# Kernel optimization log

Measured on AMD Instinct MI355X. Metric: run time of the kernel, lower is better.

The kernel has to match this reference:

```python
import jax, jax.numpy as jnp
import numpy as np

N, D, K = 131072, 128, 256
MAX_ITER = 8
TOL = 1e-4


def setup_inputs() -> dict:
    key = jax.random.key(0)
    kx, kp = jax.random.split(key)
    X = jax.random.normal(kx, (N, D), dtype=jnp.float32)
    # torch.randperm(N)[:K] -> distinct initial centroid indices
    init_idx = jax.random.permutation(kp, N)[:K]
    return {"X": X, "init_idx": init_idx, "max_iter": MAX_ITER}


def _assign(X, centroids):
    # argmin over Euclidean distance == argmin over squared distance;
    # ||x||^2 is constant per row so drop it: d2[n,k] = ||c_k||^2 - 2 x_n . c_k
    d2 = jnp.sum(centroids * centroids, axis=1)[None, :] - 2.0 * (X @ centroids.T)  # [N,K]
    return jnp.argmin(d2, axis=1)  # [N]


def reference(X, init_idx, max_iter):
    n = X.shape[0]
    centroids0 = X[init_idx]  # [K,D]

    def step(carry, _):
        centroids, done = carry
        labels = _assign(X, centroids)  # [N]
        sums = jax.ops.segment_sum(X, labels, num_segments=K)  # [K,D]
        counts = jax.ops.segment_sum(jnp.ones((n,), X.dtype), labels, num_segments=K)  # [K]
        new_c = sums / counts[:, None]  # empty cluster -> 0/0 = nan (matches torch mean of empty)
        shift = jnp.linalg.norm(new_c - centroids)
        new_done = jnp.logical_or(done, shift < TOL)
        # torch breaks BEFORE assigning new centroids when converged
        centroids = jnp.where(new_done, centroids, new_c)
        return (centroids, new_done), labels

    (centroids, _), labels_hist = jax.lax.scan(
        step, (centroids0, jnp.array(False)), None, length=max_iter
    )
    labels = labels_hist[-1]
    return labels, centroids
```

## Files before the change

### kernel.cpp

```cpp
#include <hip/hip_runtime.h>

#define NP 131072
#define DD 128
#define KK 256
#define MAXIT 8
#define TOLSQ (1e-4f * 1e-4f)
#define POSB 256
#define UPIPE 8

typedef _Float16 half8 __attribute__((ext_vector_type(8)));
typedef float f32x4 __attribute__((ext_vector_type(4)));

__device__ __forceinline__ void async_copy16(const void* g, void* l) {
    __builtin_amdgcn_global_load_lds(
        (const __attribute__((address_space(1))) void*)g,
        (__attribute__((address_space(3))) void*)l, 16, 0, 0);
}

struct Ws {
    float C[KK * DD];
    float newC[KK * DD];
    float cnorm[KK];
    float sums[KK * DD];
    float shiftsq;
    int done;
    int ilab[NP];
    int counts[KK];
    int cursor[KK];
    int ordlab[NP];
    alignas(16) _Float16 Csh[KK * DD];
    alignas(16) _Float16 Csl[KK * DD];
    alignas(16) _Float16 Xsh[(size_t)NP * DD];
    alignas(16) _Float16 Xsl[(size_t)NP * DD];
};

__global__ void k_init(const float* __restrict__ X, const int* __restrict__ idx,
                       float* __restrict__ C, int* __restrict__ done) {
    int k = blockIdx.x, d = threadIdx.x;
    C[k * DD + d] = X[(size_t)idx[k] * DD + d];
    if (k == 0 && d == 0) *done = 0;
}

__global__ void k_split(const float* __restrict__ X, _Float16* __restrict__ Xh,
                        _Float16* __restrict__ Xl) {
    size_t idx = (size_t)blockIdx.x * 256 + threadIdx.x;
    int lane = idx & 63;
    size_t g16k = idx >> 6;
    size_t point = (g16k >> 2) * 16 + (lane & 15);
    int dim0 = (int)(g16k & 3) * 32 + (lane >> 4) * 8;
    const f32x4* s4 = (const f32x4*)(X + point * DD + dim0);
    f32x4 a = s4[0], b = s4[1];
    half8 h, l;
#pragma unroll
    for (int j = 0; j < 4; j++) {
        _Float16 hi = (_Float16)a[j];
        h[j] = hi; l[j] = (_Float16)(a[j] - (float)hi);
    }
#pragma unroll
    for (int j = 0; j < 4; j++) {
        _Float16 hi = (_Float16)b[j];
        h[4 + j] = hi; l[4 + j] = (_Float16)(b[j] - (float)hi);
    }
    *(half8*)(Xh + idx * 8) = h;
    *(half8*)(Xl + idx * 8) = l;
}

__global__ void k_prep0(const float* __restrict__ C, float* __restrict__ cnorm,
                        _Float16* __restrict__ Ch, _Float16* __restrict__ Cl,
                        int* __restrict__ counts, int* __restrict__ cursor) {
    int k = blockIdx.x, d = threadIdx.x;
    float v = C[k * DD + d];
    _Float16 hi = (_Float16)v;
    int ct = k >> 4, l4 = k & 15, ks = d >> 5, q = (d >> 3) & 3, j = d & 7;
    size_t dst = ((size_t)(ks * 16 + ct) * 64 + (q * 16 + l4)) * 8 + j;
    Ch[dst] = hi;
    Cl[dst] = (_Float16)(v - (float)hi);
    __shared__ float red[DD];
    red[d] = v * v;
    __syncthreads();
    for (int s = DD / 2; s > 0; s >>= 1) {
        if (d < s) red[d] += red[d + s];
        __syncthreads();
    }
    if (d == 0) {
        cnorm[k] = red[0];
        counts[k] = 0;
        cursor[k] = 0;
    }
}

__global__ __launch_bounds__(512, 2) void k_assign(
    const _Float16* __restrict__ Xh, const _Float16* __restrict__ Xl,
    const _Float16* __restrict__ Ch, const _Float16* __restrict__ Cl,
    const float* __restrict__ cnorm, float* __restrict__ outlab,
    int* __restrict__ ilab, int* __restrict__ counts,
    float* __restrict__ shiftsq) {
    __shared__ __align__(16) _Float16 B[2 * KK * DD];
    __shared__ int hist[KK];
    const int tid = threadIdx.x;
    const int wave = tid >> 6;
    const int lane = tid & 63;
    const int l4 = lane & 15, g = lane >> 4;

    if (blockIdx.x == 0 && tid == 0) *shiftsq = 0.0f;
    if (tid < KK) hist[tid] = 0;

    char* const lds = (char*)B;
#pragma unroll
    for (int r = 0; r < 8; r++) {
        const int slot = r * 512 + wave * 64;
        async_copy16(Ch + (size_t)(slot + lane) * 8, lds + (size_t)slot * 16);
        async_copy16(Cl + (size_t)(slot + lane) * 8,
                     lds + 65536 + (size_t)slot * 16);
    }

    float cn[16];
#pragma unroll
    for (int ct = 0; ct < 16; ct++) cn[ct] = cnorm[ct * 16 + l4];

    __syncthreads();

#pragma unroll 1
    for (int t = 0; t < 2; t++) {
        const int g16 = blockIdx.x * 32 + t * 16 + wave * 2;

        f32x4 acc[2][16];
#pragma unroll
        for (int pg = 0; pg < 2; pg++)
#pragma unroll
            for (int ct = 0; ct < 16; ct++) acc[pg][ct] = (f32x4){0.f, 0.f, 0.f, 0.f};

        size_t a0 = ((size_t)(g16 * 4 + 0) * 64 + lane) * 8;
        size_t a1 = ((size_t)((g16 + 1) * 4 + 0) * 64 + lane) * 8;
        half8 ah0 = *(const half8*)(Xh + a0);
        half8 al0 = *(const half8*)(Xl + a0);
        half8 ah1 = *(const half8*)(Xh + a1);
        half8 al1 = *(const half8*)(Xl + a1);

#pragma unroll 1
        for (int ks = 0; ks < 4; ks++) {
            half8 nh0, nl0, nh1, nl1;
            if (ks < 3) {
                const size_t b0 = ((size_t)(g16 * 4 + ks + 1) * 64 + lane) * 8;
                const size_t b1 = ((size_t)((g16 + 1) * 4 + ks + 1) * 64 + lane) * 8;
                nh0 = *(const half8*)(Xh + b0);
                nl0 = *(const half8*)(Xl + b0);
                nh1 = *(const half8*)(Xh + b1);
                nl1 = *(const half8*)(Xl + b1);
            }

            char* const curh = lds + ks * 16384;
            char* const curl = lds + 65536 + ks * 16384;
#pragma unroll
            for (int ct = 0; ct < 16; ct++) {
                half8 bh = *(const half8*)(curh + ct * 1024 + lane * 16);
                half8 bl = *(const half8*)(curl + ct * 1024 + lane * 16);
                acc[0][ct] = __builtin_amdgcn_mfma_f32_16x16x32_f16(al0, bh, acc[0][ct], 0, 0, 0);
                acc[0][ct] = __builtin_amdgcn_mfma_f32_16x16x32_f16(ah0, bl, acc[0][ct], 0, 0, 0);
                acc[0][ct] = __builtin_amdgcn_mfma_f32_16x16x32_f16(ah0, bh, acc[0][ct], 0, 0, 0);
                acc[1][ct] = __builtin_amdgcn_mfma_f32_16x16x32_f16(al1, bh, acc[1][ct], 0, 0, 0);
                acc[1][ct] = __builtin_amdgcn_mfma_f32_16x16x32_f16(ah1, bl, acc[1][ct], 0, 0, 0);
                acc[1][ct] = __builtin_amdgcn_mfma_f32_16x16x32_f16(ah1, bh, acc[1][ct], 0, 0, 0);
            }
            ah0 = nh0; al0 = nl0; ah1 = nh1; al1 = nl1;
        }

        unsigned long long best[2][4];
#pragma unroll
        for (int pg = 0; pg < 2; pg++)
#pragma unroll
            for (int r = 0; r < 4; r++) best[pg][r] = ~0ull;

#pragma unroll
        for (int pg = 0; pg < 2; pg++)
#pragma unroll
            for (int ct = 0; ct < 16; ct++)
#pragma unroll
                for (int r = 0; r < 4; r++) {
                    float s = fmaf(-2.0f, acc[pg][ct][r], cn[ct]);
                    if (__builtin_isnan(s)) s = -__builtin_inff();
                    unsigned u = __float_as_uint(s);
                    unsigned m = (u >> 31) ? ~u : (u ^ 0x80000000u);
                    unsigned long long key =
                        ((unsigned long long)m << 32) | (unsigned)(ct * 16 + l4);
                    if (key < best[pg][r]) best[pg][r] = key;
                }

#pragma unroll
        for (int d = 1; d < 16; d <<= 1)
#pragma unroll
            for (int pg = 0; pg < 2; pg++)
#pragma unroll
                for (int r = 0; r < 4; r++) {
                    unsigned long long o = __shfl_xor(best[pg][r], d, 64);
                    if (o < best[pg][r]) best[pg][r] = o;
                }

        if (l4 == 0) {
#pragma unroll
            for (int pg = 0; pg < 2; pg++)
#pragma unroll
                for (int r = 0; r < 4; r++) {
                    int point = (g16 + pg) * 16 + g * 4 + r;
                    int lbl = (int)(best[pg][r] & 0x1ff);
                    outlab[point] = (float)lbl;
                    ilab[point] = lbl;
                    atomicAdd(&hist[lbl], 1);
                }
        }
    }

    __syncthreads();
    if (tid < KK) {
        int h = hist[tid];
        if (h) atomicAdd(&counts[tid], h);
    }
}

__global__ __launch_bounds__(256) void k_scatter(
    const int* __restrict__ ilab, const int* __restrict__ counts,
    int* __restrict__ cursor, int* __restrict__ ordlab,
    float* __restrict__ sums) {
    const int t = threadIdx.x;
    const int b = blockIdx.x;

    if (t < 128) sums[b * 128 + t] = 0.0f;

    __shared__ int hist[KK];
    __shared__ int pre[KK];
    __shared__ int gbase[KK];
    hist[t] = 0;
    int c = counts[t];
    pre[t] = c;
    __syncthreads();

    const int p0 = b * 512;
    const int la = ilab[p0 + t];
    const int lb = ilab[p0 + 256 + t];
    atomicAdd(&hist[la], 1);
    atomicAdd(&hist[lb], 1);

#pragma unroll
    for (int d = 1; d < KK; d <<= 1) {
        int v = (t >= d) ? pre[t - d] : 0;
        __syncthreads();
        pre[t] += v;
        __syncthreads();
    }
    int h = hist[t];
    int gb = (pre[t] - c) + (h ? atomicAdd(&cursor[t], h) : 0);
    gbase[t] = gb;
    __syncthreads();
    hist[t] = 0;
    __syncthreads();

    int ra = atomicAdd(&hist[la], 1);
    ordlab[gbase[la] + ra] = (p0 + t) | (la << 17);
    int rb = atomicAdd(&hist[lb], 1);
    ordlab[gbase[lb] + rb] = (p0 + 256 + t) | (lb << 17);
}

__global__ __launch_bounds__(256) void k_sum(
    const float* __restrict__ X, const int* __restrict__ ordlab,
    float* __restrict__ sums) {
    const int t = threadIdx.x;
    const int d = t & 127, h = t >> 7;

    __shared__ int sol[POSB];
    sol[t] = ordlab[blockIdx.x * POSB + t];
    __syncthreads();

    const int PP = POSB / 2;
    float xv[UPIPE], xn[UPIPE];
#pragma unroll
    for (int u = 0; u < UPIPE; u++)
        xv[u] = X[(size_t)(sol[2 * u + h] & 0x1ffff) * DD + d];

    float acc = 0.0f;
    int cur = sol[h] >> 17;

    for (int jb = 0; jb < PP; jb += UPIPE) {
#pragma unroll
        for (int u = 0; u < UPIPE; u++) {
            int nj = jb + u + UPIPE;
            int o = sol[2 * (nj < PP ? nj : PP - 1) + h];
            xn[u] = X[(size_t)(o & 0x1ffff) * DD + d];
        }
#pragma unroll
        for (int u = 0; u < UPIPE; u++) {
            int l = sol[2 * (jb + u) + h] >> 17;
            if (l != cur) {
                atomicAdd(&sums[cur * DD + d], acc);
                acc = 0.0f;
                cur = l;
            }
            acc += xv[u];
        }
#pragma unroll
        for (int u = 0; u < UPIPE; u++) xv[u] = xn[u];
    }
    atomicAdd(&sums[cur * DD + d], acc);
}

__global__ void k_reduce(const float* __restrict__ sums, const int* __restrict__ counts,
                         const float* __restrict__ C, float* __restrict__ newC,
                         float* __restrict__ shiftsq) {
    const int g = blockIdx.x * 256 + threadIdx.x;
    const int k = g >> 7;
    const int t = threadIdx.x;

    float nc = sums[g] / (float)counts[k];
    newC[g] = nc;
    float diff = nc - C[g];

    __shared__ float red[256];
    red[t] = diff * diff;
    __syncthreads();
    for (int st = 128; st > 0; st >>= 1) {
        if (t < st) red[t] += red[t + st];
        __syncthreads();
    }
    if (t == 0) atomicAdd(shiftsq, red[0]);
}

__global__ void k_upprep(const float* __restrict__ newC, float* __restrict__ C,
                         const float* __restrict__ shiftsq, int* __restrict__ done,
                         float* __restrict__ cnorm, _Float16* __restrict__ Ch,
                         _Float16* __restrict__ Cl, int* __restrict__ counts,
                         int* __restrict__ cursor) {
    const int t = threadIdx.x;
    const int k = blockIdx.x * 2 + (t >> 7);
    const int d = t & 127;
    float ss = *shiftsq;
    int nd = (*done != 0) || (ss < TOLSQ);
    float v = nd ? C[k * DD + d] : newC[k * DD + d];
    C[k * DD + d] = v;
    if (blockIdx.x == 0 && t == 0 && nd) *done = 1;
    if (d == 0) {
        counts[k] = 0;
        cursor[k] = 0;
    }

    _Float16 hi = (_Float16)v;
    int ct = k >> 4, l4 = k & 15, ks = d >> 5, q = (d >> 3) & 3, j = d & 7;
    size_t dst = ((size_t)(ks * 16 + ct) * 64 + (q * 16 + l4)) * 8 + j;
    Ch[dst] = hi;
    Cl[dst] = (_Float16)(v - (float)hi);

    __shared__ float red[256];
    red[t] = v * v;
    __syncthreads();
    for (int s = 64; s > 0; s >>= 1) {
        if ((t & 127) < s) red[t] += red[t + s];
        __syncthreads();
    }
    if (d == 0) cnorm[k] = red[t];
}

__global__ void k_final(const float* __restrict__ C, float* __restrict__ out) {
    int i = blockIdx.x * 256 + threadIdx.x;
    out[i] = C[i];
}

extern "C" void kernel_launch(void* const* d_in, const int* in_sizes, int n_in,
                              void* d_out, int out_size, void* d_ws, size_t ws_size,
                              hipStream_t stream) {
    const float* X = (const float*)d_in[0];
    const int* idx = (const int*)d_in[1];
    float* out = (float*)d_out;
    Ws* w = (Ws*)d_ws;

    k_init<<<KK, DD, 0, stream>>>(X, idx, w->C, &w->done);
    k_split<<<(int)((size_t)NP * DD / 8 / 256), 256, 0, stream>>>(X, w->Xsh, w->Xsl);
    k_prep0<<<KK, DD, 0, stream>>>(w->C, w->cnorm, w->Csh, w->Csl, w->counts, w->cursor);

    for (int it = 0; it < MAXIT; it++) {
        k_assign<<<NP / 512, 512, 0, stream>>>(w->Xsh, w->Xsl, w->Csh, w->Csl,
                                               w->cnorm, out, w->ilab, w->counts,
                                               &w->shiftsq);
        k_scatter<<<NP / 512, 256, 0, stream>>>(w->ilab, w->counts, w->cursor,
                                                w->ordlab, w->sums);
        k_sum<<<NP / POSB, 256, 0, stream>>>(X, w->ordlab, w->sums);
        k_reduce<<<KK * DD / 256, 256, 0, stream>>>(w->sums, w->counts, w->C,
                                                    w->newC, &w->shiftsq);
        k_upprep<<<KK / 2, 256, 0, stream>>>(w->newC, w->C, &w->shiftsq, &w->done,
                                             w->cnorm, w->Csh, w->Csl, w->counts,
                                             w->cursor);
    }

    k_final<<<KK * DD / 256, 256, 0, stream>>>(w->C, out + NP);
}
```

Baseline: 653.8 us.

## Keep centroid fragments in registers and split clusters across waves

```diff
diff --git a/kernel.cpp b/kernel.cpp
--- a/kernel.cpp
+++ b/kernel.cpp
@@ -10,12 +10,6 @@
 
 typedef _Float16 half8 __attribute__((ext_vector_type(8)));
 typedef float f32x4 __attribute__((ext_vector_type(4)));
-
-__device__ __forceinline__ void async_copy16(const void* g, void* l) {
-    __builtin_amdgcn_global_load_lds(
-        (const __attribute__((address_space(1))) void*)g,
-        (__attribute__((address_space(3))) void*)l, 16, 0, 0);
-}
 
 struct Ws {
     float C[KK * DD];
@@ -95,72 +89,71 @@
     const float* __restrict__ cnorm, float* __restrict__ outlab,
     int* __restrict__ ilab, int* __restrict__ counts,
     float* __restrict__ shiftsq) {
-    __shared__ __align__(16) _Float16 B[2 * KK * DD];
+    __shared__ unsigned long long mbuf[4][512];
     __shared__ int hist[KK];
     const int tid = threadIdx.x;
     const int wave = tid >> 6;
     const int lane = tid & 63;
     const int l4 = lane & 15, g = lane >> 4;
+    const int pgrp = wave >> 2;
+    const int q = wave & 3;
 
     if (blockIdx.x == 0 && tid == 0) *shiftsq = 0.0f;
     if (tid < KK) hist[tid] = 0;
 
-    char* const lds = (char*)B;
-#pragma unroll
+    half8 Bh[4][4], Bl[4][4];
+#pragma unroll
+    for (int ks = 0; ks < 4; ks++)
+#pragma unroll
+        for (int c = 0; c < 4; c++) {
+            size_t off = ((size_t)(ks * 16 + q * 4 + c) * 64 + lane) * 8;
+            Bh[ks][c] = *(const half8*)(Ch + off);
+            Bl[ks][c] = *(const half8*)(Cl + off);
+        }
+
+    float cn[4];
+#pragma unroll
+    for (int c = 0; c < 4; c++) cn[c] = cnorm[(q * 4 + c) * 16 + l4];
+
+    const int gb = blockIdx.x * 32 + pgrp * 2;
+    size_t a0 = ((size_t)(gb * 4) * 64 + lane) * 8;
+    size_t a1 = ((size_t)((gb + 1) * 4) * 64 + lane) * 8;
+    half8 ah0 = *(const half8*)(Xh + a0), al0 = *(const half8*)(Xl + a0);
+    half8 ah1 = *(const half8*)(Xh + a1), al1 = *(const half8*)(Xl + a1);
+
+#pragma unroll 1
     for (int r = 0; r < 8; r++) {
-        const int slot = r * 512 + wave * 64;
-        async_copy16(Ch + (size_t)(slot + lane) * 8, lds + (size_t)slot * 16);
-        async_copy16(Cl + (size_t)(slot + lane) * 8,
-                     lds + 65536 + (size_t)slot * 16);
-    }
-
-    float cn[16];
-#pragma unroll
-    for (int ct = 0; ct < 16; ct++) cn[ct] = cnorm[ct * 16 + l4];
-
-    __syncthreads();
-
-#pragma unroll 1
-    for (int t = 0; t < 2; t++) {
-        const int g16 = blockIdx.x * 32 + t * 16 + wave * 2;
-
-        f32x4 acc[2][16];
+        f32x4 acc[2][4];
 #pragma unroll
         for (int pg = 0; pg < 2; pg++)
 #pragma unroll
-            for (int ct = 0; ct < 16; ct++) acc[pg][ct] = (f32x4){0.f, 0.f, 0.f, 0.f};
-
-        size_t a0 = ((size_t)(g16 * 4 + 0) * 64 + lane) * 8;
-        size_t a1 = ((size_t)((g16 + 1) * 4 + 0) * 64 + lane) * 8;
-        half8 ah0 = *(const half8*)(Xh + a0);
-        half8 al0 = *(const half8*)(Xl + a0);
-        half8 ah1 = *(const half8*)(Xh + a1);
-        half8 al1 = *(const half8*)(Xl + a1);
-
-#pragma unroll 1
+            for (int c = 0; c < 4; c++) acc[pg][c] = (f32x4){0.f, 0.f, 0.f, 0.f};
+
+#pragma unroll
         for (int ks = 0; ks < 4; ks++) {
-            half8 nh0, nl0, nh1, nl1;
-            if (ks < 3) {
-                const size_t b0 = ((size_t)(g16 * 4 + ks + 1) * 64 + lane) * 8;
-                const size_t b1 = ((size_t)((g16 + 1) * 4 + ks + 1) * 64 + lane) * 8;
-                nh0 = *(const half8*)(Xh + b0);
-                nl0 = *(const half8*)(Xl + b0);
-                nh1 = *(const half8*)(Xh + b1);
-                nl1 = *(const half8*)(Xl + b1);
+            int ns = r * 4 + ks + 1;
+            ns = ns > 31 ? 31 : ns;
+            const int ng16 = blockIdx.x * 32 + (ns >> 2) * 4 + pgrp * 2;
+            const int nks = ns & 3;
+            const size_t b0 = ((size_t)(ng16 * 4 + nks) * 64 + lane) * 8;
+            const size_t b1 = ((size_t)((ng16 + 1) * 4 + nks) * 64 + lane) * 8;
+            half8 nh0 = *(const half8*)(Xh + b0), nl0 = *(const half8*)(Xl + b0);
+            half8 nh1 = *(const half8*)(Xh + b1), nl1 = *(const half8*)(Xl + b1);
+
+#pragma unroll
+            for (int c = 0; c < 4; c++) {
+                acc[0][c] = __builtin_amdgcn_mfma_f32_16x16x32_f16(al0, Bh[ks][c], acc[0][c], 0, 0, 0);
+                acc[1][c] = __builtin_amdgcn_mfma_f32_16x16x32_f16(al1, Bh[ks][c], acc[1][c], 0, 0, 0);
             }
-
-            char* const curh = lds + ks * 16384;
-            char* const curl = lds + 65536 + ks * 16384;
-#pragma unroll
-            for (int ct = 0; ct < 16; ct++) {
-                half8 bh = *(const half8*)(curh + ct * 1024 + lane * 16);
-                half8 bl = *(const half8*)(curl + ct * 1024 + lane * 16);
-                acc[0][ct] = __builtin_amdgcn_mfma_f32_16x16x32_f16(al0, bh, acc[0][ct], 0, 0, 0);
-                acc[0][ct] = __builtin_amdgcn_mfma_f32_16x16x32_f16(ah0, bl, acc[0][ct], 0, 0, 0);
-                acc[0][ct] = __builtin_amdgcn_mfma_f32_16x16x32_f16(ah0, bh, acc[0][ct], 0, 0, 0);
-                acc[1][ct] = __builtin_amdgcn_mfma_f32_16x16x32_f16(al1, bh, acc[1][ct], 0, 0, 0);
-                acc[1][ct] = __builtin_amdgcn_mfma_f32_16x16x32_f16(ah1, bl, acc[1][ct], 0, 0, 0);
-                acc[1][ct] = __builtin_amdgcn_mfma_f32_16x16x32_f16(ah1, bh, acc[1][ct], 0, 0, 0);
+#pragma unroll
+            for (int c = 0; c < 4; c++) {
+                acc[0][c] = __builtin_amdgcn_mfma_f32_16x16x32_f16(ah0, Bl[ks][c], acc[0][c], 0, 0, 0);
+                acc[1][c] = __builtin_amdgcn_mfma_f32_16x16x32_f16(ah1, Bl[ks][c], acc[1][c], 0, 0, 0);
+            }
+#pragma unroll
+            for (int c = 0; c < 4; c++) {
+                acc[0][c] = __builtin_amdgcn_mfma_f32_16x16x32_f16(ah0, Bh[ks][c], acc[0][c], 0, 0, 0);
+                acc[1][c] = __builtin_amdgcn_mfma_f32_16x16x32_f16(ah1, Bh[ks][c], acc[1][c], 0, 0, 0);
             }
             ah0 = nh0; al0 = nl0; ah1 = nh1; al1 = nl1;
         }
@@ -169,21 +162,22 @@
 #pragma unroll
         for (int pg = 0; pg < 2; pg++)
 #pragma unroll
-            for (int r = 0; r < 4; r++) best[pg][r] = ~0ull;
+            for (int rr = 0; rr < 4; rr++) best[pg][rr] = ~0ull;
 
 #pragma unroll
         for (int pg = 0; pg < 2; pg++)
 #pragma unroll
-            for (int ct = 0; ct < 16; ct++)
-#pragma unroll
-                for (int r = 0; r < 4; r++) {
-                    float s = fmaf(-2.0f, acc[pg][ct][r], cn[ct]);
+            for (int c = 0; c < 4; c++)
+#pragma unroll
+                for (int rr = 0; rr < 4; rr++) {
+                    float s = fmaf(-2.0f, acc[pg][c][rr], cn[c]);
                     if (__builtin_isnan(s)) s = -__builtin_inff();
                     unsigned u = __float_as_uint(s);
                     unsigned m = (u >> 31) ? ~u : (u ^ 0x80000000u);
                     unsigned long long key =
-                        ((unsigned long long)m << 32) | (unsigned)(ct * 16 + l4);
-                    if (key < best[pg][r]) best[pg][r] = key;
+                        ((unsigned long long)m << 32) |
+                        (unsigned)((q * 4 + c) * 16 + l4);
+                    if (key < best[pg][rr]) best[pg][rr] = key;
                 }
 
 #pragma unroll
@@ -191,25 +185,35 @@
 #pragma unroll
             for (int pg = 0; pg < 2; pg++)
 #pragma unroll
-                for (int r = 0; r < 4; r++) {
-                    unsigned long long o = __shfl_xor(best[pg][r], d, 64);
-                    if (o < best[pg][r]) best[pg][r] = o;
+                for (int rr = 0; rr < 4; rr++) {
+                    unsigned long long o = __shfl_xor(best[pg][rr], d, 64);
+                    if (o < best[pg][rr]) best[pg][rr] = o;
                 }
 
         if (l4 == 0) {
 #pragma unroll
             for (int pg = 0; pg < 2; pg++)
 #pragma unroll
-                for (int r = 0; r < 4; r++) {
-                    int point = (g16 + pg) * 16 + g * 4 + r;
-                    int lbl = (int)(best[pg][r] & 0x1ff);
-                    outlab[point] = (float)lbl;
-                    ilab[point] = lbl;
-                    atomicAdd(&hist[lbl], 1);
+                for (int rr = 0; rr < 4; rr++) {
+                    int pl = (r * 4 + pgrp * 2 + pg) * 16 + g * 4 + rr;
+                    mbuf[q][pl] = best[pg][rr];
                 }
         }
     }
 
+    __syncthreads();
+    {
+        unsigned long long k0 = mbuf[0][tid], k1 = mbuf[1][tid];
+        unsigned long long k2 = mbuf[2][tid], k3 = mbuf[3][tid];
+        unsigned long long ka = k0 < k1 ? k0 : k1;
+        unsigned long long kb = k2 < k3 ? k2 : k3;
+        unsigned long long k = ka < kb ? ka : kb;
+        int point = blockIdx.x * 512 + tid;
+        int lbl = (int)(k & 0x1ff);
+        outlab[point] = (float)lbl;
+        ilab[point] = lbl;
+        atomicAdd(&hist[lbl], 1);
+    }
     __syncthreads();
     if (tid < KK) {
         int h = hist[tid];
```

New measurement: 631.8 us. 3.4% less time.
